# Optimization experiments

Hardware: AMD Instinct MI355X
Metric: run time of the kernel (lower is better)

The kernel has to match this reference:

```python
import jax, jax.numpy as jnp
import numpy as np

B, F, T, N, A, E_INC, NUM_EDGES, C_OUT = 32, 64, 20, 512, 64, 2048, 128, 128
C_IN = F + A


def setup_inputs() -> dict:
    key = jax.random.key(0)
    k = jax.random.split(key, 6)
    x = jax.random.normal(k[0], (B, F, T, N), dtype=jnp.float32)
    H = jax.random.randint(k[1], (B, T, 2, E_INC), 0, NUM_EDGES)  # row0: node ids, row1: hyperedge ids
    ssa = jax.random.normal(k[2], (B, T, N, A), dtype=jnp.float32)
    W = jax.random.uniform(k[3], (B, T, E_INC), dtype=jnp.float32)  # unused by conv (matches original)
    theta = jax.random.normal(k[4], (C_OUT, C_IN), dtype=jnp.float32) / np.sqrt(C_IN).astype(np.float32)
    bias = jnp.zeros((C_OUT,), dtype=jnp.float32)
    return {"x": x, "H": H, "ssa": ssa, "W": W, "theta": theta, "bias": bias}


def _hconv(feat, hidx, theta, bias):
    # One PyG HypergraphConv (no attention, unit hyperedge weights):
    #   out = D^{-1} H B^{-1} H^T (X Theta^T) + b
    # feat: [N, C_in], hidx: [2, E_inc]
    node_idx, edge_idx = hidx[0], hidx[1]
    xp = feat @ theta.T  # [N, C_out]
    ones = jnp.ones(node_idx.shape, dtype=xp.dtype)
    deg_n = jax.ops.segment_sum(ones, node_idx, num_segments=N)         # D
    deg_e = jax.ops.segment_sum(ones, edge_idx, num_segments=NUM_EDGES)  # B
    Dinv = jnp.where(deg_n > 0, 1.0 / deg_n, 0.0)
    Binv = jnp.where(deg_e > 0, 1.0 / deg_e, 0.0)
    # node -> hyperedge aggregation
    edge_feat = Binv[:, None] * jax.ops.segment_sum(xp[node_idx], edge_idx, num_segments=NUM_EDGES)
    # hyperedge -> node aggregation
    out = Dinv[:, None] * jax.ops.segment_sum(edge_feat[edge_idx], node_idx, num_segments=N)
    return out + bias


def reference(x, H, ssa, W, theta, bias):
    # x: [B, F, T, N] -> [B, T, N, F], concat scene attention -> [B, T, N, C_in]
    feat = jnp.concatenate([jnp.transpose(x, (0, 2, 3, 1)), ssa], axis=-1)
    conv = lambda f, h: _hconv(f, h, theta, bias)
    out = jax.vmap(jax.vmap(conv))(feat, H)  # [B, T, N, C_out]
    # Original does a raw .reshape(B, C_out, T, N) (NOT a permute) -- replicate exactly.
    return out.reshape(B, C_OUT, T, N)
```

## Files before the change

### kernel.cpp

```cpp
#include <hip/hip_runtime.h>
#include <cstdint>
#include <cstddef>

namespace {

constexpr int B_ = 32, F_ = 64, T_ = 20, N_ = 512, A_ = 64;
constexpr int EINC = 2048, NEDGE = 128, COUT = 128, CIN = 128;
constexpr int THREADS = 1024;

constexpr int L_SRT8 = 0;
constexpr int L_OFN  = 512;
constexpr int L_XQ   = 1028;
constexpr int L_DGE  = 1028;
constexpr int L_CUE  = 1156;
constexpr int L_OFE  = 1284;
constexpr int L_DGN  = 1416;
constexpr int L_CUN  = 1928;
constexpr int L_ESR  = 2440;
constexpr int L_EQ   = 3464;
constexpr int L_ST   = 5512;
constexpr int XQS    = 132;
constexpr int LDS_WORDS = L_XQ + NEDGE * XQS;
constexpr int LDS_BYTES = LDS_WORDS * 4;

typedef unsigned u32x8 __attribute__((ext_vector_type(8)));
typedef float f32x4v __attribute__((ext_vector_type(4)));
typedef short bf16x8v __attribute__((ext_vector_type(8)));

__device__ inline unsigned short f2bf(float f) {
    unsigned int u = __float_as_uint(f);
    u = u + 0x7FFFu + ((u >> 16) & 1u);
    return (unsigned short)(u >> 16);
}
__device__ inline unsigned packbf(float lo, float hi) {
    return ((unsigned)f2bf(hi) << 16) | (unsigned)f2bf(lo);
}
__device__ inline float bflo(unsigned p) { return __uint_as_float(p << 16); }
__device__ inline float bfhi(unsigned p) { return __uint_as_float(p & 0xFFFF0000u); }

#define LOAD_CHUNK(CC, DST) do {                                              \
    const int c_ = (CC);                                                      \
    if (c_ < 4) {                                                             \
        const float* xr_ = x + (((size_t)b * F_ + c_ * 16) * T_ + t) * N_ + n; \
        _Pragma("unroll")                                                     \
        for (int m_ = 0; m_ < 8; ++m_) {                                      \
            float f0_ = xr_[(size_t)(2 * m_) * (T_ * N_)];                    \
            float f1_ = xr_[(size_t)(2 * m_ + 1) * (T_ * N_)];                \
            DST[m_] = packbf(f0_, f1_);                                       \
        }                                                                     \
    } else {                                                                  \
        const float* sr_ = ssa + ((size_t)bt * N_ + n) * A_ + (c_ - 4) * 16;  \
        _Pragma("unroll")                                                     \
        for (int m_ = 0; m_ < 4; ++m_) {                                      \
            float4 u_ = *(const float4*)(sr_ + 4 * m_);                       \
            DST[2 * m_]     = packbf(u_.x, u_.y);                             \
            DST[2 * m_ + 1] = packbf(u_.z, u_.w);                             \
        }                                                                     \
    }                                                                         \
} while (0)

__global__ __launch_bounds__(256)
void theta_pack(const float* __restrict__ theta, unsigned* __restrict__ ws) {
    int w = blockIdx.x * 256 + threadIdx.x;
    int f = w >> 8, rem = w & 255;
    int l = rem >> 2, kq = rem & 3;
    int kk = f & 3, ct = f >> 2;
    int co = ct * 16 + (l & 15);
    int ci = kk * 32 + (l >> 4) * 8 + kq * 2;
    const float2 tv = *(const float2*)(theta + (size_t)co * CIN + ci);
    ws[w] = packbf(tv.x, tv.y);
}

template<bool HAS_WS>
__global__ __launch_bounds__(THREADS, 8)
void hgconv(const float* __restrict__ x, const int* __restrict__ H,
            const float* __restrict__ ssa, const float* __restrict__ theta,
            const float* __restrict__ bias, float* __restrict__ out,
            const unsigned* __restrict__ thw)
{
    extern __shared__ float sf[];
    int* si = (int*)sf;

    const int tid = (int)threadIdx.x;
    const int bt  = (int)blockIdx.x;
    const int b   = bt / T_;
    const int t   = bt - b * T_;

    unsigned char*  s_srt8  = (unsigned char*)(si + L_SRT8);
    int*            s_ofn   = si + L_OFN;
    int*            s_ofe   = si + L_OFE;
    int*            s_dge   = si + L_DGE;
    int*            s_cue   = si + L_CUE;
    int*            s_dgn   = si + L_DGN;
    int*            s_cun   = si + L_CUN;
    unsigned short* s_esr16 = (unsigned short*)(si + L_ESR);
    unsigned*       s_eq16  = (unsigned*)(si + L_EQ);
    unsigned*       s_st16  = (unsigned*)(si + L_ST);
    int*            s_nid   = si + L_EQ;
    int*            s_eid   = si + L_ST;
    float*          s_xq    = sf + L_XQ;

    const int n  = tid & (N_ - 1);
    const int hf = tid >> 9;

    const int* Hb = H + (size_t)bt * (2 * EINC);
    #pragma unroll
    for (int k = 0; k < EINC / THREADS; ++k) {
        int i = tid + k * THREADS;
        s_nid[i] = Hb[i];
        s_eid[i] = Hb[EINC + i];
    }
    if (tid < N_)    s_dgn[tid] = 0;
    if (tid < NEDGE) s_dge[tid] = 0;
    __syncthreads();

    #pragma unroll
    for (int k = 0; k < EINC / THREADS; ++k) {
        int i = tid + k * THREADS;
        atomicAdd(&s_dgn[s_nid[i]], 1);
        atomicAdd(&s_dge[s_eid[i]], 1);
    }
    __syncthreads();

    const bool act = s_dgn[n] > 0;
    u32x8 vv;
    if (act) LOAD_CHUNK(hf, vv);

    if (tid < 64) {
        const int l = tid;
        int d0 = s_dge[2 * l], d1 = s_dge[2 * l + 1];
        int run = d0 + d1;
        int scan = run;
        #pragma unroll
        for (int d = 1; d < 64; d <<= 1) {
            int o = __shfl_up(scan, d);
            if (l >= d) scan += o;
        }
        int excl = scan - run;
        s_ofe[2 * l] = excl;
        s_ofe[2 * l + 1] = excl + d0;
        if (l == 63) s_ofe[NEDGE] = scan;
    } else if (tid < 128) {
        const int l = tid & 63;
        int v, loc[8], run = 0;
        #pragma unroll
        for (int q = 0; q < 8; ++q) { v = s_dgn[l * 8 + q]; loc[q] = run; run += v; }
        int scan = run;
        #pragma unroll
        for (int d = 1; d < 64; d <<= 1) {
            int o = __shfl_up(scan, d);
            if (l >= d) scan += o;
        }
        int excl = scan - run;
        #pragma unroll
        for (int q = 0; q < 8; ++q) s_ofn[l * 8 + q] = excl + loc[q];
        if (l == 63) s_ofn[N_] = scan;
    }
    __syncthreads();

    if (tid < N_)    s_cun[tid] = s_ofn[tid];
    if (tid < NEDGE) s_cue[tid] = s_ofe[tid];
    __syncthreads();

    #pragma unroll
    for (int k = 0; k < EINC / THREADS; ++k) {
        int i = tid + k * THREADS;
        int nd = s_nid[i];
        int e  = s_eid[i];
        int pe = atomicAdd(&s_cue[e], 1);
        s_esr16[pe] = (unsigned short)nd;
        int pn = atomicAdd(&s_cun[nd], 1);
        s_srt8[pn] = (unsigned char)e;
    }
    __syncthreads();

    const int eg = tid >> 3;
    const int ep = tid & 7;
    const int wv = tid >> 6, l = tid & 63;
    const int q  = l >> 4, lco = l & 15;
    const int rt = wv >> 1;
    const int cth = (wv & 1) * 4;
    const int ar = rt * 16 + lco;
    const int aoff = ar * 16 + ((4 * q) ^ ((ar & 3) << 2));
    const int k0 = s_ofe[eg], k1 = s_ofe[eg + 1];
    const float binv = (k1 > k0) ? 1.0f / (float)(k1 - k0) : 0.0f;

    f32x4v acc[4];
    #pragma unroll
    for (int i = 0; i < 4; ++i) acc[i] = (f32x4v){0.f, 0.f, 0.f, 0.f};

    #pragma unroll
    for (int r = 0; r < 4; ++r) {
        if (act) {
            #pragma unroll
            for (int p2 = 0; p2 < 4; ++p2) {
                int P = 4 * hf + p2;
                unsigned* sp = s_st16 + n * 16 + ((2 * P) ^ ((n & 7) << 1));
                *(uint2*)sp = make_uint2(vv[2 * p2], vv[2 * p2 + 1]);
            }
        }
        __syncthreads();

        if (r < 3 && act) LOAD_CHUNK(2 * r + 2 + hf, vv);

        {
            float a0 = 0.f, a1 = 0.f, a2 = 0.f, a3 = 0.f;
            for (int k = k0; k < k1; ++k) {
                int nd = (int)s_esr16[k];
                uint2 pr = *(const uint2*)(s_st16 + nd * 16
                                + ((2 * ep) ^ ((nd & 7) << 1)));
                a0 += bflo(pr.x); a1 += bfhi(pr.x);
                a2 += bflo(pr.y); a3 += bfhi(pr.y);
            }
            unsigned* qp = s_eq16 + eg * 16 + ((2 * ep) ^ ((eg & 3) << 2));
            *(uint2*)qp = make_uint2(packbf(a0 * binv, a1 * binv),
                                     packbf(a2 * binv, a3 * binv));
        }
        __syncthreads();

        {
            bf16x8v av = *(const bf16x8v*)(s_eq16 + aoff);
            if (HAS_WS) {
                #pragma unroll
                for (int i = 0; i < 4; ++i) {
                    uint4 u = ((const uint4*)thw)[((cth + i) * 4 + r) * 64 + l];
                    acc[i] = __builtin_amdgcn_mfma_f32_16x16x32_bf16(
                        av, *(const bf16x8v*)&u, acc[i], 0, 0, 0);
                }
            } else {
                #pragma unroll
                for (int i = 0; i < 4; ++i) {
                    const float* tp = theta + (size_t)((cth + i) * 16 + lco) * CIN
                                    + r * 32 + q * 8;
                    float4 t0 = *(const float4*)tp;
                    float4 t1 = *(const float4*)(tp + 4);
                    unsigned pw[4] = { packbf(t0.x, t0.y), packbf(t0.z, t0.w),
                                       packbf(t1.x, t1.y), packbf(t1.z, t1.w) };
                    acc[i] = __builtin_amdgcn_mfma_f32_16x16x32_bf16(
                        av, *(const bf16x8v*)pw, acc[i], 0, 0, 0);
                }
            }
        }
    }
    __syncthreads();

    #pragma unroll
    for (int i = 0; i < 4; ++i) {
        const int co = (cth + i) * 16 + lco;
        #pragma unroll
        for (int reg = 0; reg < 4; ++reg)
            s_xq[(rt * 16 + q * 4 + reg) * XQS + co] = acc[i][reg];
    }
    __syncthreads();

    {
        const int lw = tid & 31;
        const int g  = tid >> 5;
        float4 bsv = *(const float4*)(bias + 4 * lw);
        for (int nn = g; nn < N_; nn += 32) {
            int o0 = s_ofn[nn], o1 = s_ofn[nn + 1];
            float f0 = 0.f, f1 = 0.f, f2 = 0.f, f3 = 0.f;
            for (int k = o0; k < o1; ++k) {
                int e = (int)s_srt8[k];
                float4 v = *(const float4*)(s_xq + e * XQS + 4 * lw);
                f0 += v.x; f1 += v.y; f2 += v.z; f3 += v.w;
            }
            float dinv = (o1 > o0) ? 1.0f / (float)(o1 - o0) : 0.0f;
            float* op = out + ((size_t)bt * N_ + nn) * COUT + 4 * lw;
            *(float4*)op = make_float4(f0 * dinv + bsv.x, f1 * dinv + bsv.y,
                                       f2 * dinv + bsv.z, f3 * dinv + bsv.w);
        }
    }
}

}

extern "C" void kernel_launch(void* const* d_in, const int* in_sizes, int n_in,
                              void* d_out, int out_size, void* d_ws, size_t ws_size,
                              hipStream_t stream) {
    const float* x     = (const float*)d_in[0];
    const int*   H     = (const int*)d_in[1];
    const float* ssa   = (const float*)d_in[2];
    const float* theta = (const float*)d_in[4];
    const float* bias  = (const float*)d_in[5];
    float* outp = (float*)d_out;

    const bool use_ws = (d_ws != nullptr) && (ws_size >= 32768);
    if (use_ws) {
        hipLaunchKernelGGL(theta_pack, dim3(32), dim3(256), 0, stream,
                           theta, (unsigned*)d_ws);
        (void)hipFuncSetAttribute((const void*)&hgconv<true>,
                                  hipFuncAttributeMaxDynamicSharedMemorySize, LDS_BYTES);
        hipLaunchKernelGGL(hgconv<true>, dim3(B_ * T_), dim3(THREADS), LDS_BYTES,
                           stream, x, H, ssa, theta, bias, outp,
                           (const unsigned*)d_ws);
    } else {
        (void)hipFuncSetAttribute((const void*)&hgconv<false>,
                                  hipFuncAttributeMaxDynamicSharedMemorySize, LDS_BYTES);
        hipLaunchKernelGGL(hgconv<false>, dim3(B_ * T_), dim3(THREADS), LDS_BYTES,
                           stream, x, H, ssa, theta, bias, outp, nullptr);
    }
}
```

Before: 81.95 us.

## Use persistent blocks with an atomic work queue over batch-time slices

The main kernel now launches a fixed grid of 512 blocks instead of 640. Each block loops, taking its next (b,t) slice from a global atomic counter that theta_pack initializes in the workspace. The aim is to avoid a partial second wave of 1024-thread blocks and balance uneven per-slice work across CUs. This adds an atomic and two barriers per slice, and later slices get no overlap with the previous slice's tail.

```diff
diff --git a/kernel.cpp b/kernel.cpp
--- a/kernel.cpp
+++ b/kernel.cpp
@@ -7,9 +7,12 @@
 constexpr int B_ = 32, F_ = 64, T_ = 20, N_ = 512, A_ = 64;
 constexpr int EINC = 2048, NEDGE = 128, COUT = 128, CIN = 128;
 constexpr int THREADS = 1024;
+constexpr int NBT = B_ * T_;
+constexpr int GRID_WS = 512;
 
 constexpr int L_SRT8 = 0;
 constexpr int L_OFN  = 512;
+constexpr int L_NXT  = 1026;
 constexpr int L_XQ   = 1028;
 constexpr int L_DGE  = 1028;
 constexpr int L_CUE  = 1156;
@@ -69,6 +72,7 @@
     int ci = kk * 32 + (l >> 4) * 8 + kq * 2;
     const float2 tv = *(const float2*)(theta + (size_t)co * CIN + ci);
     ws[w] = packbf(tv.x, tv.y);
+    if (w == 0) ws[8192] = (unsigned)GRID_WS;
 }
 
 template<bool HAS_WS>
@@ -76,15 +80,12 @@
 void hgconv(const float* __restrict__ x, const int* __restrict__ H,
             const float* __restrict__ ssa, const float* __restrict__ theta,
             const float* __restrict__ bias, float* __restrict__ out,
-            const unsigned* __restrict__ thw)
+            const unsigned* __restrict__ thw, unsigned* __restrict__ wq)
 {
     extern __shared__ float sf[];
     int* si = (int*)sf;
 
     const int tid = (int)threadIdx.x;
-    const int bt  = (int)blockIdx.x;
-    const int b   = bt / T_;
-    const int t   = bt - b * T_;
 
     unsigned char*  s_srt8  = (unsigned char*)(si + L_SRT8);
     int*            s_ofn   = si + L_OFN;
@@ -103,77 +104,6 @@
     const int n  = tid & (N_ - 1);
     const int hf = tid >> 9;
 
-    const int* Hb = H + (size_t)bt * (2 * EINC);
-    #pragma unroll
-    for (int k = 0; k < EINC / THREADS; ++k) {
-        int i = tid + k * THREADS;
-        s_nid[i] = Hb[i];
-        s_eid[i] = Hb[EINC + i];
-    }
-    if (tid < N_)    s_dgn[tid] = 0;
-    if (tid < NEDGE) s_dge[tid] = 0;
-    __syncthreads();
-
-    #pragma unroll
-    for (int k = 0; k < EINC / THREADS; ++k) {
-        int i = tid + k * THREADS;
-        atomicAdd(&s_dgn[s_nid[i]], 1);
-        atomicAdd(&s_dge[s_eid[i]], 1);
-    }
-    __syncthreads();
-
-    const bool act = s_dgn[n] > 0;
-    u32x8 vv;
-    if (act) LOAD_CHUNK(hf, vv);
-
-    if (tid < 64) {
-        const int l = tid;
-        int d0 = s_dge[2 * l], d1 = s_dge[2 * l + 1];
-        int run = d0 + d1;
-        int scan = run;
-        #pragma unroll
-        for (int d = 1; d < 64; d <<= 1) {
-            int o = __shfl_up(scan, d);
-            if (l >= d) scan += o;
-        }
-        int excl = scan - run;
-        s_ofe[2 * l] = excl;
-        s_ofe[2 * l + 1] = excl + d0;
-        if (l == 63) s_ofe[NEDGE] = scan;
-    } else if (tid < 128) {
-        const int l = tid & 63;
-        int v, loc[8], run = 0;
-        #pragma unroll
-        for (int q = 0; q < 8; ++q) { v = s_dgn[l * 8 + q]; loc[q] = run; run += v; }
-        int scan = run;
-        #pragma unroll
-        for (int d = 1; d < 64; d <<= 1) {
-            int o = __shfl_up(scan, d);
-            if (l >= d) scan += o;
-        }
-        int excl = scan - run;
-        #pragma unroll
-        for (int q = 0; q < 8; ++q) s_ofn[l * 8 + q] = excl + loc[q];
-        if (l == 63) s_ofn[N_] = scan;
-    }
-    __syncthreads();
-
-    if (tid < N_)    s_cun[tid] = s_ofn[tid];
-    if (tid < NEDGE) s_cue[tid] = s_ofe[tid];
-    __syncthreads();
-
-    #pragma unroll
-    for (int k = 0; k < EINC / THREADS; ++k) {
-        int i = tid + k * THREADS;
-        int nd = s_nid[i];
-        int e  = s_eid[i];
-        int pe = atomicAdd(&s_cue[e], 1);
-        s_esr16[pe] = (unsigned short)nd;
-        int pn = atomicAdd(&s_cun[nd], 1);
-        s_srt8[pn] = (unsigned char)e;
-    }
-    __syncthreads();
-
     const int eg = tid >> 3;
     const int ep = tid & 7;
     const int wv = tid >> 6, l = tid & 63;
@@ -182,94 +112,181 @@
     const int cth = (wv & 1) * 4;
     const int ar = rt * 16 + lco;
     const int aoff = ar * 16 + ((4 * q) ^ ((ar & 3) << 2));
-    const int k0 = s_ofe[eg], k1 = s_ofe[eg + 1];
-    const float binv = (k1 > k0) ? 1.0f / (float)(k1 - k0) : 0.0f;
-
-    f32x4v acc[4];
-    #pragma unroll
-    for (int i = 0; i < 4; ++i) acc[i] = (f32x4v){0.f, 0.f, 0.f, 0.f};
-
-    #pragma unroll
-    for (int r = 0; r < 4; ++r) {
-        if (act) {
-            #pragma unroll
-            for (int p2 = 0; p2 < 4; ++p2) {
-                int P = 4 * hf + p2;
-                unsigned* sp = s_st16 + n * 16 + ((2 * P) ^ ((n & 7) << 1));
-                *(uint2*)sp = make_uint2(vv[2 * p2], vv[2 * p2 + 1]);
-            }
-        }
-        __syncthreads();
-
-        if (r < 3 && act) LOAD_CHUNK(2 * r + 2 + hf, vv);
+
+    int bt = (int)blockIdx.x;
+
+    for (;;) {
+        const int b = bt / T_;
+        const int t = bt - b * T_;
+
+        const int* Hb = H + (size_t)bt * (2 * EINC);
+        #pragma unroll
+        for (int k = 0; k < EINC / THREADS; ++k) {
+            int i = tid + k * THREADS;
+            s_nid[i] = Hb[i];
+            s_eid[i] = Hb[EINC + i];
+        }
+        if (tid < N_)    s_dgn[tid] = 0;
+        if (tid < NEDGE) s_dge[tid] = 0;
+        __syncthreads();
+
+        #pragma unroll
+        for (int k = 0; k < EINC / THREADS; ++k) {
+            int i = tid + k * THREADS;
+            atomicAdd(&s_dgn[s_nid[i]], 1);
+            atomicAdd(&s_dge[s_eid[i]], 1);
+        }
+        __syncthreads();
+
+        const bool act = s_dgn[n] > 0;
+        u32x8 vv;
+        if (act) LOAD_CHUNK(hf, vv);
+
+        if (tid < 64) {
+            const int ll = tid;
+            int d0 = s_dge[2 * ll], d1 = s_dge[2 * ll + 1];
+            int run = d0 + d1;
+            int scan = run;
+            #pragma unroll
+            for (int d = 1; d < 64; d <<= 1) {
+                int o = __shfl_up(scan, d);
+                if (ll >= d) scan += o;
+            }
+            int excl = scan - run;
+            s_ofe[2 * ll] = excl;
+            s_ofe[2 * ll + 1] = excl + d0;
+            if (ll == 63) s_ofe[NEDGE] = scan;
+        } else if (tid < 128) {
+            const int ll = tid & 63;
+            int v, loc[8], run = 0;
+            #pragma unroll
+            for (int qq = 0; qq < 8; ++qq) { v = s_dgn[ll * 8 + qq]; loc[qq] = run; run += v; }
+            int scan = run;
+            #pragma unroll
+            for (int d = 1; d < 64; d <<= 1) {
+                int o = __shfl_up(scan, d);
+                if (ll >= d) scan += o;
+            }
+            int excl = scan - run;
+            #pragma unroll
+            for (int qq = 0; qq < 8; ++qq) s_ofn[ll * 8 + qq] = excl + loc[qq];
+            if (ll == 63) s_ofn[N_] = scan;
+        }
+        __syncthreads();
+
+        if (tid < N_)    s_cun[tid] = s_ofn[tid];
+        if (tid < NEDGE) s_cue[tid] = s_ofe[tid];
+        __syncthreads();
+
+        #pragma unroll
+        for (int k = 0; k < EINC / THREADS; ++k) {
+            int i = tid + k * THREADS;
+            int nd = s_nid[i];
+            int e  = s_eid[i];
+            int pe = atomicAdd(&s_cue[e], 1);
+            s_esr16[pe] = (unsigned short)nd;
+            int pn = atomicAdd(&s_cun[nd], 1);
+            s_srt8[pn] = (unsigned char)e;
+        }
+        __syncthreads();
+
+        const int k0 = s_ofe[eg], k1 = s_ofe[eg + 1];
+        const float binv = (k1 > k0) ? 1.0f / (float)(k1 - k0) : 0.0f;
+
+        f32x4v acc[4];
+        #pragma unroll
+        for (int i = 0; i < 4; ++i) acc[i] = (f32x4v){0.f, 0.f, 0.f, 0.f};
+
+        #pragma unroll
+        for (int r = 0; r < 4; ++r) {
+            if (act) {
+                #pragma unroll
+                for (int p2 = 0; p2 < 4; ++p2) {
+                    int P = 4 * hf + p2;
+                    unsigned* sp = s_st16 + n * 16 + ((2 * P) ^ ((n & 7) << 1));
+                    *(uint2*)sp = make_uint2(vv[2 * p2], vv[2 * p2 + 1]);
+                }
+            }
+            __syncthreads();
+
+            if (r < 3 && act) LOAD_CHUNK(2 * r + 2 + hf, vv);
+
+            {
+                float a0 = 0.f, a1 = 0.f, a2 = 0.f, a3 = 0.f;
+                for (int k = k0; k < k1; ++k) {
+                    int nd = (int)s_esr16[k];
+                    uint2 pr = *(const uint2*)(s_st16 + nd * 16
+                                    + ((2 * ep) ^ ((nd & 7) << 1)));
+                    a0 += bflo(pr.x); a1 += bfhi(pr.x);
+                    a2 += bflo(pr.y); a3 += bfhi(pr.y);
+                }
+                unsigned* qp = s_eq16 + eg * 16 + ((2 * ep) ^ ((eg & 3) << 2));
+                *(uint2*)qp = make_uint2(packbf(a0 * binv, a1 * binv),
+                                         packbf(a2 * binv, a3 * binv));
+            }
+            __syncthreads();
+
+            {
+                bf16x8v av = *(const bf16x8v*)(s_eq16 + aoff);
+                if (HAS_WS) {
+                    #pragma unroll
+                    for (int i = 0; i < 4; ++i) {
+                        uint4 u = ((const uint4*)thw)[((cth + i) * 4 + r) * 64 + l];
+                        acc[i] = __builtin_amdgcn_mfma_f32_16x16x32_bf16(
+                            av, *(const bf16x8v*)&u, acc[i], 0, 0, 0);
+                    }
+                } else {
+                    #pragma unroll
+                    for (int i = 0; i < 4; ++i) {
+                        const float* tp = theta + (size_t)((cth + i) * 16 + lco) * CIN
+                                        + r * 32 + q * 8;
+                        float4 t0 = *(const float4*)tp;
+                        float4 t1 = *(const float4*)(tp + 4);
+                        unsigned pw[4] = { packbf(t0.x, t0.y), packbf(t0.z, t0.w),
+                                           packbf(t1.x, t1.y), packbf(t1.z, t1.w) };
+                        acc[i] = __builtin_amdgcn_mfma_f32_16x16x32_bf16(
+                            av, *(const bf16x8v*)pw, acc[i], 0, 0, 0);
+                    }
+                }
+            }
+        }
+        __syncthreads();
+
+        #pragma unroll
+        for (int i = 0; i < 4; ++i) {
+            const int co = (cth + i) * 16 + lco;
+            #pragma unroll
+            for (int reg = 0; reg < 4; ++reg)
+                s_xq[(rt * 16 + q * 4 + reg) * XQS + co] = acc[i][reg];
+        }
+        __syncthreads();
 
         {
-            float a0 = 0.f, a1 = 0.f, a2 = 0.f, a3 = 0.f;
-            for (int k = k0; k < k1; ++k) {
-                int nd = (int)s_esr16[k];
-                uint2 pr = *(const uint2*)(s_st16 + nd * 16
-                                + ((2 * ep) ^ ((nd & 7) << 1)));
-                a0 += bflo(pr.x); a1 += bfhi(pr.x);
-                a2 += bflo(pr.y); a3 += bfhi(pr.y);
-            }
-            unsigned* qp = s_eq16 + eg * 16 + ((2 * ep) ^ ((eg & 3) << 2));
-            *(uint2*)qp = make_uint2(packbf(a0 * binv, a1 * binv),
-                                     packbf(a2 * binv, a3 * binv));
-        }
-        __syncthreads();
-
-        {
-            bf16x8v av = *(const bf16x8v*)(s_eq16 + aoff);
-            if (HAS_WS) {
-                #pragma unroll
-                for (int i = 0; i < 4; ++i) {
-                    uint4 u = ((const uint4*)thw)[((cth + i) * 4 + r) * 64 + l];
-                    acc[i] = __builtin_amdgcn_mfma_f32_16x16x32_bf16(
-                        av, *(const bf16x8v*)&u, acc[i], 0, 0, 0);
+            const int lw = tid & 31;
+            const int g  = tid >> 5;
+            float4 bsv = *(const float4*)(bias + 4 * lw);
+            for (int nn = g; nn < N_; nn += 32) {
+                int o0 = s_ofn[nn], o1 = s_ofn[nn + 1];
+                float f0 = 0.f, f1 = 0.f, f2 = 0.f, f3 = 0.f;
+                for (int k = o0; k < o1; ++k) {
+                    int e = (int)s_srt8[k];
+                    float4 v = *(const float4*)(s_xq + e * XQS + 4 * lw);
+                    f0 += v.x; f1 += v.y; f2 += v.z; f3 += v.w;
                 }
-            } else {
-                #pragma unroll
-                for (int i = 0; i < 4; ++i) {
-                    const float* tp = theta + (size_t)((cth + i) * 16 + lco) * CIN
-                                    + r * 32 + q * 8;
-                    float4 t0 = *(const float4*)tp;
-                    float4 t1 = *(const float4*)(tp + 4);
-                    unsigned pw[4] = { packbf(t0.x, t0.y), packbf(t0.z, t0.w),
-                                       packbf(t1.x, t1.y), packbf(t1.z, t1.w) };
-                    acc[i] = __builtin_amdgcn_mfma_f32_16x16x32_bf16(
-                        av, *(const bf16x8v*)pw, acc[i], 0, 0, 0);
-                }
-            }
-        }
-    }
-    __syncthreads();
-
-    #pragma unroll
-    for (int i = 0; i < 4; ++i) {
-        const int co = (cth + i) * 16 + lco;
-        #pragma unroll
-        for (int reg = 0; reg < 4; ++reg)
-            s_xq[(rt * 16 + q * 4 + reg) * XQS + co] = acc[i][reg];
-    }
-    __syncthreads();
-
-    {
-        const int lw = tid & 31;
-        const int g  = tid >> 5;
-        float4 bsv = *(const float4*)(bias + 4 * lw);
-        for (int nn = g; nn < N_; nn += 32) {
-            int o0 = s_ofn[nn], o1 = s_ofn[nn + 1];
-            float f0 = 0.f, f1 = 0.f, f2 = 0.f, f3 = 0.f;
-            for (int k = o0; k < o1; ++k) {
-                int e = (int)s_srt8[k];
-                float4 v = *(const float4*)(s_xq + e * XQS + 4 * lw);
-                f0 += v.x; f1 += v.y; f2 += v.z; f3 += v.w;
-            }
-            float dinv = (o1 > o0) ? 1.0f / (float)(o1 - o0) : 0.0f;
-            float* op = out + ((size_t)bt * N_ + nn) * COUT + 4 * lw;
-            *(float4*)op = make_float4(f0 * dinv + bsv.x, f1 * dinv + bsv.y,
-                                       f2 * dinv + bsv.z, f3 * dinv + bsv.w);
-        }
+                float dinv = (o1 > o0) ? 1.0f / (float)(o1 - o0) : 0.0f;
+                float* op = out + ((size_t)bt * N_ + nn) * COUT + 4 * lw;
+                *(float4*)op = make_float4(f0 * dinv + bsv.x, f1 * dinv + bsv.y,
+                                           f2 * dinv + bsv.z, f3 * dinv + bsv.w);
+            }
+        }
+
+        if (!HAS_WS) break;
+
+        __syncthreads();
+        if (tid == 0) si[L_NXT] = (int)atomicAdd(wq, 1u);
+        __syncthreads();
+        bt = si[L_NXT];
+        if (bt >= NBT) break;
     }
 }
 
@@ -285,19 +302,19 @@
     const float* bias  = (const float*)d_in[5];
     float* outp = (float*)d_out;
 
-    const bool use_ws = (d_ws != nullptr) && (ws_size >= 32768);
+    const bool use_ws = (d_ws != nullptr) && (ws_size >= 32772);
     if (use_ws) {
         hipLaunchKernelGGL(theta_pack, dim3(32), dim3(256), 0, stream,
                            theta, (unsigned*)d_ws);
         (void)hipFuncSetAttribute((const void*)&hgconv<true>,
                                   hipFuncAttributeMaxDynamicSharedMemorySize, LDS_BYTES);
-        hipLaunchKernelGGL(hgconv<true>, dim3(B_ * T_), dim3(THREADS), LDS_BYTES,
+        hipLaunchKernelGGL(hgconv<true>, dim3(GRID_WS), dim3(THREADS), LDS_BYTES,
                            stream, x, H, ssa, theta, bias, outp,
-                           (const unsigned*)d_ws);
+                           (const unsigned*)d_ws, (unsigned*)d_ws + 8192);
     } else {
         (void)hipFuncSetAttribute((const void*)&hgconv<false>,
                                   hipFuncAttributeMaxDynamicSharedMemorySize, LDS_BYTES);
-        hipLaunchKernelGGL(hgconv<false>, dim3(B_ * T_), dim3(THREADS), LDS_BYTES,
-                           stream, x, H, ssa, theta, bias, outp, nullptr);
+        hipLaunchKernelGGL(hgconv<false>, dim3(NBT), dim3(THREADS), LDS_BYTES,
+                           stream, x, H, ssa, theta, bias, outp, nullptr, nullptr);
     }
 }
```

Result: slower. 160.4 us (+95.7%).
